# Kernel tuning notes

Hardware: AMD Instinct MI355X
Metric: run time of the kernel (lower is better)

Reference implementation:

```python
import jax, jax.numpy as jnp
import numpy as np

N_NODES = 500_000
N_EDGES = 16_000_000


def setup_inputs() -> dict:
    key = jax.random.key(0)
    ks = jax.random.split(key, 16)
    x = jax.random.normal(ks[0], (N_NODES, 4), dtype=jnp.float32)
    edge_index = jax.random.randint(ks[1], (2, N_EDGES), 0, N_NODES, dtype=jnp.int64)

    def lin(k, out_dim, in_dim):
        # kaiming-uniform-ish init like torch Linear
        bound = 1.0 / np.sqrt(in_dim)
        return jax.random.uniform(k, (out_dim, in_dim), jnp.float32, -bound, bound)

    def bias(k, out_dim, in_dim):
        bound = 1.0 / np.sqrt(in_dim)
        return jax.random.uniform(k, (out_dim,), jnp.float32, -bound, bound)

    return {
        "x": x,
        "edge_index": edge_index,
        # SAGEConv1: 4 -> 10  (lin_l acts on aggregated neighbors, has bias; lin_r on self, no bias)
        "w1l": lin(ks[2], 10, 4), "b1": bias(ks[3], 10, 4), "w1r": lin(ks[4], 10, 4),
        # SAGEConv2: 10 -> 20
        "w2l": lin(ks[5], 20, 10), "b2": bias(ks[6], 20, 10), "w2r": lin(ks[7], 20, 10),
        # SAGEConv3: 20 -> 20
        "w3l": lin(ks[8], 20, 20), "b3": bias(ks[9], 20, 20), "w3r": lin(ks[10], 20, 20),
        # classifier: 20 -> 8
        "wc": lin(ks[11], 8, 20), "bc": bias(ks[12], 8, 20),
    }


def _sage_conv(h, src, dst, deg_inv, wl, bl, wr):
    # mean-aggregate neighbor features: messages flow src -> dst
    msg = h[src]                                   # [E, F] gather
    agg = jax.ops.segment_sum(msg, dst, num_segments=N_NODES)  # [N, F]
    agg = agg * deg_inv                            # mean over in-neighbors
    return agg @ wl.T + bl + h @ wr.T              # lin_l(aggr) + lin_r(self)


def reference(x, edge_index, w1l, b1, w1r, w2l, b2, w2r, w3l, b3, w3r, wc, bc):
    src, dst = edge_index[0], edge_index[1]
    deg = jax.ops.segment_sum(jnp.ones((src.shape[0],), x.dtype), dst,
                              num_segments=N_NODES)
    deg_inv = (1.0 / jnp.maximum(deg, 1.0))[:, None]  # [N, 1]

    h = jax.nn.relu(_sage_conv(x, src, dst, deg_inv, w1l, b1, w1r))
    h = jax.nn.relu(_sage_conv(h, src, dst, deg_inv, w2l, b2, w2r))
    h = jax.nn.relu(_sage_conv(h, src, dst, deg_inv, w3l, b3, w3r))
    return h @ wc.T + bc
```

## Files before the change

kernel.cpp:

```cpp
#include <hip/hip_runtime.h>
#include <hip/hip_fp16.h>

#define N_NODES 500000
#define N_EDGES 16000000
#define NB 1954
#define NPB_LOG 9
#define NPB 512
#define NBUCK 977
#define NBUCK_PAD 1024
#define CH 32768
#define NSB 489

#define SLICE_SHIFT 15
#define NSLICE 16
#define NKEY (NPB * NSLICE)

#define GRID_BLK 1024
#define HALF_T (GRID_BLK * 256)

#define BAR_SUBC 16
#define BAR_SUBQ (GRID_BLK / BAR_SUBC)
#define BAR_REC_INTS 1024
#define BAR_MASTER 512
#define BAR_FLAG 544
#define ENTRY_BUDGET 1500
#define PHASE_BUDGET 400

__device__ __forceinline__ float2 up2(int p) {
    __half2 h = *reinterpret_cast<__half2*>(&p);
    return __half22float2(h);
}
__device__ __forceinline__ int pk2(float a, float b) {
    __half2 h = __floats2half2_rn(a, b);
    return *reinterpret_cast<int*>(&h);
}

__device__ __forceinline__ void barrier_arrive(int* rec, int bid) {
    int r = __hip_atomic_fetch_add(&rec[(bid & (BAR_SUBC - 1)) * 32], 1,
                                   __ATOMIC_RELAXED, __HIP_MEMORY_SCOPE_AGENT);
    if (r == BAR_SUBQ - 1) {
        int mr = __hip_atomic_fetch_add(&rec[BAR_MASTER], 1,
                                        __ATOMIC_RELAXED, __HIP_MEMORY_SCOPE_AGENT);
        if (mr == BAR_SUBC - 1)
            __hip_atomic_store(&rec[BAR_FLAG], 1,
                               __ATOMIC_RELAXED, __HIP_MEMORY_SCOPE_AGENT);
    }
}
__device__ __forceinline__ bool barrier_wait(int* rec, int budget) {
    int spins = 0;
    while (__hip_atomic_load(&rec[BAR_FLAG],
                             __ATOMIC_RELAXED, __HIP_MEMORY_SCOPE_AGENT) == 0) {
        if (++spins > budget) return false;
        __builtin_amdgcn_s_sleep(8);
    }
    return true;
}


__global__ void bucket_hist(const int* __restrict__ dst, int* __restrict__ ghist) {
    __shared__ int lhist[NBUCK_PAD];
    for (int t = threadIdx.x; t < NBUCK_PAD; t += 256) lhist[t] = 0;
    __syncthreads();
    int stride = gridDim.x * 256;
    for (int i = blockIdx.x * 256 + threadIdx.x; i < N_EDGES; i += stride) {
        atomicAdd(&lhist[dst[i] >> NPB_LOG], 1);
    }
    __syncthreads();
    for (int t = threadIdx.x; t < NBUCK_PAD; t += 256) {
        int c = lhist[t];
        if (c) atomicAdd(&ghist[t], c);
    }
}

__global__ void bucket_scan(int* __restrict__ gcur, int* __restrict__ bbase) {
    __shared__ int s[256];
    int t = threadIdx.x;
    int v[4], sum = 0, loc[4];
#pragma unroll
    for (int j = 0; j < 4; ++j) {
        v[j] = gcur[t * 4 + j];
        loc[j] = sum;
        sum += v[j];
    }
    s[t] = sum;
    __syncthreads();
    for (int o = 1; o < 256; o <<= 1) {
        int x = (t >= o) ? s[t - o] : 0;
        __syncthreads();
        s[t] += x;
        __syncthreads();
    }
    int excl = s[t] - sum;
#pragma unroll
    for (int j = 0; j < 4; ++j) {
        int e = excl + loc[j];
        bbase[t * 4 + j] = e;
        gcur[t * 4 + j] = e;
    }
    if (t == 255) bbase[NBUCK_PAD] = s[255];
}

__global__ void bucket_scatter(const int* __restrict__ src, const int* __restrict__ dst,
                               int* __restrict__ gcur, int* __restrict__ P) {
    __shared__ int lhist[NBUCK_PAD];
    __shared__ int lcur[NBUCK_PAD];
    for (int t = threadIdx.x; t < NBUCK_PAD; t += 256) lhist[t] = 0;
    __syncthreads();
    int e0 = blockIdx.x * CH;
    int e1 = min(e0 + CH, N_EDGES);
    for (int i = e0 + threadIdx.x; i < e1; i += 256) {
        atomicAdd(&lhist[dst[i] >> NPB_LOG], 1);
    }
    __syncthreads();
    for (int t = threadIdx.x; t < NBUCK_PAD; t += 256) {
        int c = lhist[t];
        lcur[t] = c ? atomicAdd(&gcur[t], c) : 0;
    }
    __syncthreads();
    for (int i = e0 + threadIdx.x; i < e1; i += 256) {
        int d = dst[i];
        int s = src[i];
        int b = d >> NPB_LOG;
        int pos = atomicAdd(&lcur[b], 1);
        P[pos] = ((d & (NPB - 1)) << 19) | s;
    }
}

__global__ void fine_sort(const int* __restrict__ P, const int* __restrict__ bbase,
                          int* __restrict__ off, int* __restrict__ S) {
    __shared__ int hist[NKEY];
    __shared__ int sscan[256];
    int t = threadIdx.x;
    int b = blockIdx.x;
    int bb = bbase[b];
    int be = bbase[b + 1];
    int node0 = b << NPB_LOG;

    for (int j = t; j < NKEY; j += 256) hist[j] = 0;
    __syncthreads();
    for (int j = bb + t; j < be; j += 256) {
        int p = P[j];
        int n = p >> 19;
        int s = p & 0x7FFFF;
        atomicAdd(&hist[(n << 4) | (s >> SLICE_SHIFT)], 1);
    }
    __syncthreads();

    int base = t * 32;
    int sum = 0;
#pragma unroll
    for (int j = 0; j < 32; ++j) sum += hist[base + j];
    sscan[t] = sum;
    __syncthreads();
    for (int o = 1; o < 256; o <<= 1) {
        int x = (t >= o) ? sscan[t - o] : 0;
        __syncthreads();
        sscan[t] += x;
        __syncthreads();
    }
    int run = sscan[t] - sum;
#pragma unroll
    for (int j = 0; j < 32; ++j) {
        int c = hist[base + j];
        hist[base + j] = run;
        run += c;
    }
    __syncthreads();

#pragma unroll
    for (int j = 0; j < 2; ++j) {
        int idx = t + j * 256;
        int ng = node0 + idx;
        if (ng < N_NODES) off[ng] = bb + hist[idx << 4];
    }
    if (b == NBUCK - 1 && t == 0) off[N_NODES] = N_EDGES;
    __syncthreads();

    for (int j = bb + t; j < be; j += 256) {
        int p = P[j];
        int n = p >> 19;
        int s = p & 0x7FFFF;
        int pos = atomicAdd(&hist[(n << 4) | (s >> SLICE_SHIFT)], 1);
        S[bb + pos] = s;
    }
}

__global__ __launch_bounds__(256) void count_slices(const int* __restrict__ off,
        const int* __restrict__ S, int4* __restrict__ cnt8) {
    int i = blockIdx.x * 256 + threadIdx.x;
    if (i >= N_NODES) return;
    int b = off[i], e = off[i + 1];
    int w0 = 0, w1 = 0, w2 = 0, w3 = 0;
    for (int k = b; k < e; ++k) {
        int sl = S[k] >> SLICE_SHIFT;
        int inc = 1 << ((sl & 3) * 8);
        if (sl < 8) { if (sl < 4) w0 += inc; else w1 += inc; }
        else        { if (sl < 12) w2 += inc; else w3 += inc; }
    }
    cnt8[i] = make_int4(w0, w1, w2, w3);
}


__global__ void convert_x(const float* __restrict__ x, int2* __restrict__ xh) {
    int i = blockIdx.x * 256 + threadIdx.x;
    if (i >= N_NODES) return;
    float4 v = ((const float4*)x)[i];
    int2 r;
    r.x = pk2(v.x, v.y);
    r.y = pk2(v.z, v.w);
    xh[i] = r;
}


__global__ __launch_bounds__(256, 4) void fused_l1(
        const int* __restrict__ off, const int* __restrict__ ssrc,
        const int2* __restrict__ xh, const float* __restrict__ x,
        const float* __restrict__ wl, const float* __restrict__ bl,
        const float* __restrict__ wr, int* __restrict__ h1) {
    __shared__ float s_wl[40];
    __shared__ float s_wr[40];
    __shared__ float s_b[10];
    if (threadIdx.x < 40) {
        s_wl[threadIdx.x] = wl[threadIdx.x];
        s_wr[threadIdx.x] = wr[threadIdx.x];
    }
    if (threadIdx.x >= 64 && threadIdx.x < 74) s_b[threadIdx.x - 64] = bl[threadIdx.x - 64];
    __syncthreads();

    int i = blockIdx.x * 256 + threadIdx.x;
    if (i >= N_NODES) return;

    int b = off[i], e = off[i + 1];
    constexpr int UN = 8;

    float acc[4] = {0.f, 0.f, 0.f, 0.f};

    int k = b;
    for (; k + UN - 1 < e; k += UN) {
        int sidx[UN];
#pragma unroll
        for (int u = 0; u < UN; ++u) sidx[u] = ssrc[k + u];
        int2 v[UN];
#pragma unroll
        for (int u = 0; u < UN; ++u) v[u] = xh[sidx[u]];
#pragma unroll
        for (int u = 0; u < UN; ++u) {
            float2 f0 = up2(v[u].x), f1 = up2(v[u].y);
            acc[0] += f0.x; acc[1] += f0.y; acc[2] += f1.x; acc[3] += f1.y;
        }
    }
    for (; k < e; ++k) {
        int2 v = xh[ssrc[k]];
        float2 f0 = up2(v.x), f1 = up2(v.y);
        acc[0] += f0.x; acc[1] += f0.y; acc[2] += f1.x; acc[3] += f1.y;
    }

    float inv = 1.f / fmaxf((float)(e - b), 1.f);
#pragma unroll
    for (int q = 0; q < 4; ++q) acc[q] *= inv;

    float4 xs = ((const float4*)x)[i];
    float xv[4] = {xs.x, xs.y, xs.z, xs.w};

    float r[10];
#pragma unroll
    for (int j = 0; j < 10; ++j) {
        float t = s_b[j];
#pragma unroll
        for (int kk = 0; kk < 4; ++kk) {
            t += s_wl[j * 4 + kk] * acc[kk] + s_wr[j * 4 + kk] * xv[kk];
        }
        r[j] = fmaxf(t, 0.f);
    }
    int4 o0;
    o0.x = pk2(r[0], r[1]); o0.y = pk2(r[2], r[3]);
    o0.z = pk2(r[4], r[5]); o0.w = pk2(r[6], r[7]);
    *(int4*)(h1 + (long)i * 8) = o0;
    h1[(long)i * 8 + 4] = pk2(r[8], r[9]);
}


__device__ __forceinline__ void l2_scan_m(int& k, int m,
        const int* __restrict__ ssrc, const int* __restrict__ h1, float* acc) {
    for (; m >= 4; m -= 4, k += 4) {
        int sidx[4];
#pragma unroll
        for (int u = 0; u < 4; ++u) sidx[u] = ssrc[k + u];
        int4 v4[4];
        int v1[4];
#pragma unroll
        for (int u = 0; u < 4; ++u) {
            const int* row = h1 + (long)sidx[u] * 8;
            v4[u] = *(const int4*)row;
            v1[u] = row[4];
        }
#pragma unroll
        for (int u = 0; u < 4; ++u) {
            float2 f0 = up2(v4[u].x), f1 = up2(v4[u].y), f2 = up2(v4[u].z),
                   f3 = up2(v4[u].w), f4 = up2(v1[u]);
            acc[0] += f0.x; acc[1] += f0.y; acc[2] += f1.x; acc[3] += f1.y;
            acc[4] += f2.x; acc[5] += f2.y; acc[6] += f3.x; acc[7] += f3.y;
            acc[8] += f4.x; acc[9] += f4.y;
        }
    }
    for (; m > 0; --m, ++k) {
        const int* row = h1 + (long)ssrc[k] * 8;
        int4 v4 = *(const int4*)row;
        int v1 = row[4];
        float2 f0 = up2(v4.x), f1 = up2(v4.y), f2 = up2(v4.z), f3 = up2(v4.w), f4 = up2(v1);
        acc[0] += f0.x; acc[1] += f0.y; acc[2] += f1.x; acc[3] += f1.y;
        acc[4] += f2.x; acc[5] += f2.y; acc[6] += f3.x; acc[7] += f3.y;
        acc[8] += f4.x; acc[9] += f4.y;
    }
}

__device__ __forceinline__ void l3_scan_m(int& k, int m,
        const int* __restrict__ ssrc, const int* __restrict__ h2, float* acc) {
    for (; m >= 4; m -= 4, k += 4) {
        int sidx[4];
#pragma unroll
        for (int u = 0; u < 4; ++u) sidx[u] = ssrc[k + u];
        int4 va[4], vb[4];
        int2 vc[4];
#pragma unroll
        for (int u = 0; u < 4; ++u) {
            const int* row = h2 + (long)sidx[u] * 16;
            va[u] = *(const int4*)row;
            vb[u] = *(const int4*)(row + 4);
            vc[u] = *(const int2*)(row + 8);
        }
#pragma unroll
        for (int u = 0; u < 4; ++u) {
            float2 f;
            f = up2(va[u].x); acc[0] += f.x; acc[1] += f.y;
            f = up2(va[u].y); acc[2] += f.x; acc[3] += f.y;
            f = up2(va[u].z); acc[4] += f.x; acc[5] += f.y;
            f = up2(va[u].w); acc[6] += f.x; acc[7] += f.y;
            f = up2(vb[u].x); acc[8] += f.x; acc[9] += f.y;
            f = up2(vb[u].y); acc[10] += f.x; acc[11] += f.y;
            f = up2(vb[u].z); acc[12] += f.x; acc[13] += f.y;
            f = up2(vb[u].w); acc[14] += f.x; acc[15] += f.y;
            f = up2(vc[u].x); acc[16] += f.x; acc[17] += f.y;
            f = up2(vc[u].y); acc[18] += f.x; acc[19] += f.y;
        }
    }
    for (; m > 0; --m, ++k) {
        const int* row = h2 + (long)ssrc[k] * 16;
        int4 va = *(const int4*)row;
        int4 vb = *(const int4*)(row + 4);
        int2 vc = *(const int2*)(row + 8);
        float2 f;
        f = up2(va.x); acc[0] += f.x; acc[1] += f.y;
        f = up2(va.y); acc[2] += f.x; acc[3] += f.y;
        f = up2(va.z); acc[4] += f.x; acc[5] += f.y;
        f = up2(va.w); acc[6] += f.x; acc[7] += f.y;
        f = up2(vb.x); acc[8] += f.x; acc[9] += f.y;
        f = up2(vb.y); acc[10] += f.x; acc[11] += f.y;
        f = up2(vb.z); acc[12] += f.x; acc[13] += f.y;
        f = up2(vb.w); acc[14] += f.x; acc[15] += f.y;
        f = up2(vc.x); acc[16] += f.x; acc[17] += f.y;
        f = up2(vc.y); acc[18] += f.x; acc[19] += f.y;
    }
}

__device__ __forceinline__ void l2_tail(int n, float deg, float* acc,
        const int* __restrict__ h1, const float* s_wl, const float* s_wr,
        const float* s_b, int* __restrict__ h2) {
    if (n >= N_NODES) return;
    float inv = 1.f / fmaxf(deg, 1.f);
#pragma unroll
    for (int q = 0; q < 10; ++q) acc[q] *= inv;
    float xv[10];
    {
        const int* row = h1 + (long)n * 8;
        int4 v4 = *(const int4*)row;
        int v1 = row[4];
        float2 f0 = up2(v4.x), f1 = up2(v4.y), f2 = up2(v4.z), f3 = up2(v4.w), f4 = up2(v1);
        xv[0] = f0.x; xv[1] = f0.y; xv[2] = f1.x; xv[3] = f1.y;
        xv[4] = f2.x; xv[5] = f2.y; xv[6] = f3.x; xv[7] = f3.y;
        xv[8] = f4.x; xv[9] = f4.y;
    }
    float r[20];
#pragma unroll
    for (int j = 0; j < 20; ++j) {
        float t = s_b[j];
#pragma unroll
        for (int kk = 0; kk < 10; ++kk)
            t += s_wl[j * 10 + kk] * acc[kk] + s_wr[j * 10 + kk] * xv[kk];
        r[j] = fmaxf(t, 0.f);
    }
    int* o = h2 + (long)n * 16;
    int4 o0, o1;
    o0.x = pk2(r[0], r[1]);   o0.y = pk2(r[2], r[3]);
    o0.z = pk2(r[4], r[5]);   o0.w = pk2(r[6], r[7]);
    o1.x = pk2(r[8], r[9]);   o1.y = pk2(r[10], r[11]);
    o1.z = pk2(r[12], r[13]); o1.w = pk2(r[14], r[15]);
    *(int4*)o = o0;
    *(int4*)(o + 4) = o1;
    int2 o2;
    o2.x = pk2(r[16], r[17]); o2.y = pk2(r[18], r[19]);
    *(int2*)(o + 8) = o2;
}

__global__ __launch_bounds__(256, 4) void fused_l2p(
        const int* __restrict__ off, const int* __restrict__ ssrc,
        const int* __restrict__ h1,
        const float* __restrict__ wl, const float* __restrict__ bl,
        const float* __restrict__ wr, int* __restrict__ h2,
        const int4* __restrict__ cnt8, int* __restrict__ bar) {
    __shared__ float s_wl[200];
    __shared__ float s_wr[200];
    __shared__ float s_b[20];
    if (threadIdx.x < 200) {
        s_wl[threadIdx.x] = wl[threadIdx.x];
        s_wr[threadIdx.x] = wr[threadIdx.x];
    }
    if (threadIdx.x >= 224 && threadIdx.x < 244) s_b[threadIdx.x - 224] = bl[threadIdx.x - 224];
    __syncthreads();

    const int tg = blockIdx.x * 256 + threadIdx.x;
    const int n0 = tg, n1 = tg + HALF_T;
    int k0 = off[n0];
    float deg0 = (float)(off[n0 + 1] - k0);
    int4 c0 = cnt8[n0];
    int k1 = 0;
    float deg1 = 0.f;
    int4 c1 = make_int4(0, 0, 0, 0);
    if (n1 < N_NODES) {
        k1 = off[n1];
        deg1 = (float)(off[n1 + 1] - k1);
        c1 = cnt8[n1];
    }
    float acc0[10], acc1[10];
#pragma unroll
    for (int q = 0; q < 10; ++q) { acc0[q] = 0.f; acc1[q] = 0.f; }

    bool coop = true;
    if (threadIdx.x == 0) {
        barrier_arrive(bar, blockIdx.x);
        coop = barrier_wait(bar, ENTRY_BUDGET);
    }
    __syncthreads();

    constexpr int PH = 8;
    for (int s = 0; s < PH; ++s) {
        int cw0 = (s < 4) ? ((s < 2) ? c0.x : c0.y) : ((s < 6) ? c0.z : c0.w);
        int cw1 = (s < 4) ? ((s < 2) ? c1.x : c1.y) : ((s < 6) ? c1.z : c1.w);
        int sh = (s & 1) * 16;
        int m0 = ((cw0 >> sh) & 255) + ((cw0 >> (sh + 8)) & 255);
        int m1 = ((cw1 >> sh) & 255) + ((cw1 >> (sh + 8)) & 255);
        l2_scan_m(k0, m0, ssrc, h1, acc0);
        l2_scan_m(k1, m1, ssrc, h1, acc1);
        if (s < PH - 1) {
            if (threadIdx.x == 0) {
                int* rec = bar + (1 + s) * BAR_REC_INTS;
                barrier_arrive(rec, blockIdx.x);
                if (coop) coop = barrier_wait(rec, PHASE_BUDGET);
            }
            __syncthreads();
        }
    }
    l2_tail(n0, deg0, acc0, h1, s_wl, s_wr, s_b, h2);
    l2_tail(n1, deg1, acc1, h1, s_wl, s_wr, s_b, h2);
}

__device__ __forceinline__ void l3_tail(int n, float deg, float* acc,
        const int* __restrict__ h2, const float* s_wl, const float* s_wr,
        const float* s_b, const float* s_wc, const float* s_bc,
        float* __restrict__ out) {
    if (n >= N_NODES) return;
    float inv = 1.f / fmaxf(deg, 1.f);
#pragma unroll
    for (int q = 0; q < 20; ++q) acc[q] *= inv;
    float xv[20];
    {
        const int* row = h2 + (long)n * 16;
        int4 va = *(const int4*)row;
        int4 vb = *(const int4*)(row + 4);
        int2 vc = *(const int2*)(row + 8);
        float2 f;
        f = up2(va.x); xv[0] = f.x; xv[1] = f.y;
        f = up2(va.y); xv[2] = f.x; xv[3] = f.y;
        f = up2(va.z); xv[4] = f.x; xv[5] = f.y;
        f = up2(va.w); xv[6] = f.x; xv[7] = f.y;
        f = up2(vb.x); xv[8] = f.x; xv[9] = f.y;
        f = up2(vb.y); xv[10] = f.x; xv[11] = f.y;
        f = up2(vb.z); xv[12] = f.x; xv[13] = f.y;
        f = up2(vb.w); xv[14] = f.x; xv[15] = f.y;
        f = up2(vc.x); xv[16] = f.x; xv[17] = f.y;
        f = up2(vc.y); xv[18] = f.x; xv[19] = f.y;
    }
    float h3[20];
#pragma unroll
    for (int j = 0; j < 20; ++j) {
        float r = s_b[j];
#pragma unroll
        for (int kk = 0; kk < 20; ++kk)
            r += s_wl[j * 20 + kk] * acc[kk] + s_wr[j * 20 + kk] * xv[kk];
        h3[j] = fmaxf(r, 0.f);
    }
#pragma unroll
    for (int j = 0; j < 8; ++j) {
        float r = s_bc[j];
#pragma unroll
        for (int kk = 0; kk < 20; ++kk) r += s_wc[j * 20 + kk] * h3[kk];
        out[(long)n * 8 + j] = r;
    }
}

__global__ __launch_bounds__(256, 4) void fused_l3p(
        const int* __restrict__ off, const int* __restrict__ ssrc,
        const int* __restrict__ h2,
        const float* __restrict__ w3l, const float* __restrict__ b3,
        const float* __restrict__ w3r,
        const float* __restrict__ wc, const float* __restrict__ bc,
        float* __restrict__ out, const int4* __restrict__ cnt8,
        int* __restrict__ bar) {
    __shared__ float s_wl[400];
    __shared__ float s_wr[400];
    __shared__ float s_b[20];
    __shared__ float s_wc[160];
    __shared__ float s_bc[8];
    for (int t = threadIdx.x; t < 400; t += 256) {
        s_wl[t] = w3l[t];
        s_wr[t] = w3r[t];
    }
    if (threadIdx.x < 160) s_wc[threadIdx.x] = wc[threadIdx.x];
    if (threadIdx.x >= 192 && threadIdx.x < 212) s_b[threadIdx.x - 192] = b3[threadIdx.x - 192];
    if (threadIdx.x >= 224 && threadIdx.x < 232) s_bc[threadIdx.x - 224] = bc[threadIdx.x - 224];
    __syncthreads();

    const int tg = blockIdx.x * 256 + threadIdx.x;
    const int n0 = tg, n1 = tg + HALF_T;
    int k0 = off[n0];
    float deg0 = (float)(off[n0 + 1] - k0);
    int4 c0 = cnt8[n0];
    int k1 = 0;
    float deg1 = 0.f;
    int4 c1 = make_int4(0, 0, 0, 0);
    if (n1 < N_NODES) {
        k1 = off[n1];
        deg1 = (float)(off[n1 + 1] - k1);
        c1 = cnt8[n1];
    }
    float acc0[20], acc1[20];
#pragma unroll
    for (int q = 0; q < 20; ++q) { acc0[q] = 0.f; acc1[q] = 0.f; }

    bool coop = true;
    if (threadIdx.x == 0) {
        barrier_arrive(bar, blockIdx.x);
        coop = barrier_wait(bar, ENTRY_BUDGET);
    }
    __syncthreads();

    constexpr int PH = 16;
    for (int s = 0; s < PH; ++s) {
        int cw0 = (s < 8) ? ((s < 4) ? c0.x : c0.y) : ((s < 12) ? c0.z : c0.w);
        int cw1 = (s < 8) ? ((s < 4) ? c1.x : c1.y) : ((s < 12) ? c1.z : c1.w);
        int sh = (s & 3) * 8;
        int m0 = (cw0 >> sh) & 255;
        int m1 = (cw1 >> sh) & 255;
        l3_scan_m(k0, m0, ssrc, h2, acc0);
        l3_scan_m(k1, m1, ssrc, h2, acc1);
        if (s < PH - 1) {
            if (threadIdx.x == 0) {
                int* rec = bar + (1 + s) * BAR_REC_INTS;
                barrier_arrive(rec, blockIdx.x);
                if (coop) coop = barrier_wait(rec, PHASE_BUDGET);
            }
            __syncthreads();
        }
    }
    l3_tail(n0, deg0, acc0, h2, s_wl, s_wr, s_b, s_wc, s_bc, out);
    l3_tail(n1, deg1, acc1, h2, s_wl, s_wr, s_b, s_wc, s_bc, out);
}


__global__ void deg_kernel(const int* __restrict__ dst, int* __restrict__ deg) {
    int i = blockIdx.x * blockDim.x + threadIdx.x;
    if (i < N_EDGES) atomicAdd(&deg[dst[i]], 1);
}

template <int F>
__global__ void edge_agg(const int* __restrict__ src, const int* __restrict__ dst,
                         const float* __restrict__ h, float* __restrict__ agg) {
    int i = blockIdx.x * blockDim.x + threadIdx.x;
    if (i >= N_EDGES) return;
    int s = src[i];
    int d = dst[i];
    const float* hs = h + (long)s * F;
    float* ad = agg + (long)d * F;
#pragma unroll
    for (int f = 0; f < F; ++f) atomicAdd(&ad[f], hs[f]);
}

template <int FIN, int FOUT>
__global__ void node_apply(const float* __restrict__ agg, const float* __restrict__ hin,
                           const int* __restrict__ deg, const float* __restrict__ wl,
                           const float* __restrict__ bl, const float* __restrict__ wr,
                           float* __restrict__ hout) {
    __shared__ float s_wl[FOUT * FIN];
    __shared__ float s_wr[FOUT * FIN];
    __shared__ float s_b[FOUT];
    for (int t = threadIdx.x; t < FOUT * FIN; t += blockDim.x) {
        s_wl[t] = wl[t];
        s_wr[t] = wr[t];
    }
    for (int t = threadIdx.x; t < FOUT; t += blockDim.x) s_b[t] = bl[t];
    __syncthreads();
    int i = blockIdx.x * blockDim.x + threadIdx.x;
    if (i >= N_NODES) return;
    float inv = 1.0f / fmaxf((float)deg[i], 1.0f);
    float a[FIN], xv[FIN];
#pragma unroll
    for (int kk = 0; kk < FIN; ++kk) {
        a[kk] = agg[(long)i * FIN + kk] * inv;
        xv[kk] = hin[(long)i * FIN + kk];
    }
#pragma unroll
    for (int j = 0; j < FOUT; ++j) {
        float r = s_b[j];
#pragma unroll
        for (int kk = 0; kk < FIN; ++kk) r += s_wl[j * FIN + kk] * a[kk] + s_wr[j * FIN + kk] * xv[kk];
        hout[(long)i * FOUT + j] = fmaxf(r, 0.f);
    }
}

__global__ void node_final_old(const float* __restrict__ agg, const float* __restrict__ hin,
                               const int* __restrict__ deg, const float* __restrict__ w3l,
                               const float* __restrict__ b3, const float* __restrict__ w3r,
                               const float* __restrict__ wc, const float* __restrict__ bc,
                               float* __restrict__ out) {
    __shared__ float s_wl[400];
    __shared__ float s_wr[400];
    __shared__ float s_b[20];
    __shared__ float s_wc[160];
    __shared__ float s_bc[8];
    for (int t = threadIdx.x; t < 400; t += blockDim.x) {
        s_wl[t] = w3l[t];
        s_wr[t] = w3r[t];
    }
    for (int t = threadIdx.x; t < 160; t += blockDim.x) s_wc[t] = wc[t];
    for (int t = threadIdx.x; t < 20; t += blockDim.x) s_b[t] = b3[t];
    for (int t = threadIdx.x; t < 8; t += blockDim.x) s_bc[t] = bc[t];
    __syncthreads();
    int i = blockIdx.x * blockDim.x + threadIdx.x;
    if (i >= N_NODES) return;
    float inv = 1.0f / fmaxf((float)deg[i], 1.0f);
    float a[20], xv[20];
#pragma unroll
    for (int kk = 0; kk < 20; ++kk) {
        a[kk] = agg[(long)i * 20 + kk] * inv;
        xv[kk] = hin[(long)i * 20 + kk];
    }
    float h3[20];
#pragma unroll
    for (int j = 0; j < 20; ++j) {
        float r = s_b[j];
#pragma unroll
        for (int kk = 0; kk < 20; ++kk) r += s_wl[j * 20 + kk] * a[kk] + s_wr[j * 20 + kk] * xv[kk];
        h3[j] = fmaxf(r, 0.f);
    }
#pragma unroll
    for (int j = 0; j < 8; ++j) {
        float r = s_bc[j];
#pragma unroll
        for (int kk = 0; kk < 20; ++kk) r += s_wc[j * 20 + kk] * h3[kk];
        out[(long)i * 8 + j] = r;
    }
}


extern "C" void kernel_launch(void* const* d_in, const int* in_sizes, int n_in,
                              void* d_out, int out_size, void* d_ws, size_t ws_size,
                              hipStream_t stream) {
    const float* x = (const float*)d_in[0];
    const int* ei = (const int*)d_in[1];
    const float* w1l = (const float*)d_in[2];
    const float* b1 = (const float*)d_in[3];
    const float* w1r = (const float*)d_in[4];
    const float* w2l = (const float*)d_in[5];
    const float* b2 = (const float*)d_in[6];
    const float* w2r = (const float*)d_in[7];
    const float* w3l = (const float*)d_in[8];
    const float* b3 = (const float*)d_in[9];
    const float* w3r = (const float*)d_in[10];
    const float* wc = (const float*)d_in[11];
    const float* bc = (const float*)d_in[12];
    float* out = (float*)d_out;

    const int* src = ei;
    const int* dst = ei + N_EDGES;

    const int BT = 256;
    dim3 blk(BT);
    dim3 egrid((N_EDGES + BT - 1) / BT);
    dim3 ngrid(NB);

    const size_t NEED_A = 130008448;

    if (ws_size >= NEED_A) {
        char* ws = (char*)d_ws;
        int* off = (int*)ws;
        int* bbase = (int*)(ws + 2000128);
        int* gcur = (int*)(ws + 2004352);
        int* P = (int*)(ws + 2008448);
        int2* xh = (int2*)(ws + 2008448);
        int* h1 = (int*)(ws + 6008448);
        int* h2 = (int*)(ws + 22008448);
        int* bar2 = (int*)(ws + 54008448);
        int* bar3 = bar2 + 8 * BAR_REC_INTS;
        int4* cnt8 = (int4*)(ws + 54206464);
        int* S = (int*)(ws + 66008448);

        hipMemsetAsync(gcur, 0, NBUCK_PAD * sizeof(int), stream);
        bucket_hist<<<1024, blk, 0, stream>>>(dst, gcur);
        bucket_scan<<<1, blk, 0, stream>>>(gcur, bbase);
        bucket_scatter<<<NSB, blk, 0, stream>>>(src, dst, gcur, P);
        fine_sort<<<NBUCK, blk, 0, stream>>>(P, bbase, off, S);

        hipMemsetAsync(bar2, 0, 24 * BAR_REC_INTS * sizeof(int), stream);

        count_slices<<<ngrid, blk, 0, stream>>>(off, S, cnt8);
        convert_x<<<ngrid, blk, 0, stream>>>(x, xh);
        fused_l1<<<ngrid, blk, 0, stream>>>(off, S, xh, x, w1l, b1, w1r, h1);
        fused_l2p<<<GRID_BLK, blk, 0, stream>>>(off, S, h1, w2l, b2, w2r, h2, cnt8, bar2);
        fused_l3p<<<GRID_BLK, blk, 0, stream>>>(off, S, h2, w3l, b3, w3r, wc, bc, out, cnt8, bar3);
    } else {
        char* ws = (char*)d_ws;
        int* deg = (int*)ws;
        float* agg = (float*)(ws + 2000000);
        float* h1 = (float*)(ws + 42000000);
        float* h2 = (float*)(ws + 62000000);

        hipMemsetAsync(deg, 0, (size_t)N_NODES * sizeof(int), stream);
        deg_kernel<<<egrid, blk, 0, stream>>>(dst, deg);

        hipMemsetAsync(agg, 0, (size_t)N_NODES * 4 * sizeof(float), stream);
        edge_agg<4><<<egrid, blk, 0, stream>>>(src, dst, x, agg);
        node_apply<4, 10><<<ngrid, blk, 0, stream>>>(agg, x, deg, w1l, b1, w1r, h1);

        hipMemsetAsync(agg, 0, (size_t)N_NODES * 10 * sizeof(float), stream);
        edge_agg<10><<<egrid, blk, 0, stream>>>(src, dst, h1, agg);
        node_apply<10, 20><<<ngrid, blk, 0, stream>>>(agg, h1, deg, w2l, b2, w2r, h2);

        hipMemsetAsync(agg, 0, (size_t)N_NODES * 20 * sizeof(float), stream);
        edge_agg<20><<<egrid, blk, 0, stream>>>(src, dst, h2, agg);
        node_final_old<<<ngrid, blk, 0, stream>>>(agg, h2, deg, w3l, b3, w3r, wc, bc, out);
    }
}
```

Before: 1.587 ms.

## Stage bucket scatter in LDS and write contiguous per-bucket runs to global

The bucket scatter kernel now sorts each chunk's edges locally in shared memory, using a block-wide prefix scan over the bucket histogram, and then copies each bucket's run to global memory with one wavefront per bucket. The goal is to replace random 4-byte global writes with mostly contiguous writes. To fit the 64KB staging buffer, the chunk size is halved, which doubles the block count and the number of global atomics on bucket cursors. Runs average only about 16 elements per bucket, so coalescing gains may be limited, and the large LDS footprint lowers occupancy.

```diff
diff --git a/kernel.cpp b/kernel.cpp
--- a/kernel.cpp
+++ b/kernel.cpp
@@ -8,8 +8,8 @@
 #define NPB 512
 #define NBUCK 977
 #define NBUCK_PAD 1024
-#define CH 32768
-#define NSB 489
+#define CH 16384
+#define NSB 977
 
 #define SLICE_SHIFT 15
 #define NSLICE 16
@@ -100,29 +100,67 @@
     if (t == 255) bbase[NBUCK_PAD] = s[255];
 }
 
-__global__ void bucket_scatter(const int* __restrict__ src, const int* __restrict__ dst,
-                               int* __restrict__ gcur, int* __restrict__ P) {
+__global__ __launch_bounds__(256) void bucket_scatter(
+        const int* __restrict__ src, const int* __restrict__ dst,
+        int* __restrict__ gcur, int* __restrict__ P) {
+    __shared__ int lP[CH];
     __shared__ int lhist[NBUCK_PAD];
-    __shared__ int lcur[NBUCK_PAD];
-    for (int t = threadIdx.x; t < NBUCK_PAD; t += 256) lhist[t] = 0;
-    __syncthreads();
+    __shared__ int lexcl[NBUCK_PAD];
+    __shared__ int gbase[NBUCK_PAD];
+    __shared__ int sscan[256];
+    int t = threadIdx.x;
+    for (int j = t; j < NBUCK_PAD; j += 256) lhist[j] = 0;
+    __syncthreads();
+
     int e0 = blockIdx.x * CH;
     int e1 = min(e0 + CH, N_EDGES);
-    for (int i = e0 + threadIdx.x; i < e1; i += 256) {
+    for (int i = e0 + t; i < e1; i += 256) {
         atomicAdd(&lhist[dst[i] >> NPB_LOG], 1);
     }
     __syncthreads();
-    for (int t = threadIdx.x; t < NBUCK_PAD; t += 256) {
-        int c = lhist[t];
-        lcur[t] = c ? atomicAdd(&gcur[t], c) : 0;
-    }
-    __syncthreads();
-    for (int i = e0 + threadIdx.x; i < e1; i += 256) {
+
+    int base4 = t * 4;
+    int c[4], sum = 0;
+#pragma unroll
+    for (int j = 0; j < 4; ++j) { c[j] = lhist[base4 + j]; sum += c[j]; }
+#pragma unroll
+    for (int j = 0; j < 4; ++j) {
+        gbase[base4 + j] = c[j] ? atomicAdd(&gcur[base4 + j], c[j]) : 0;
+    }
+    sscan[t] = sum;
+    __syncthreads();
+    for (int o = 1; o < 256; o <<= 1) {
+        int x = (t >= o) ? sscan[t - o] : 0;
+        __syncthreads();
+        sscan[t] += x;
+        __syncthreads();
+    }
+    int run = sscan[t] - sum;
+#pragma unroll
+    for (int j = 0; j < 4; ++j) {
+        lexcl[base4 + j] = run;
+        lhist[base4 + j] = run;
+        run += c[j];
+    }
+    __syncthreads();
+
+    for (int i = e0 + t; i < e1; i += 256) {
         int d = dst[i];
         int s = src[i];
         int b = d >> NPB_LOG;
-        int pos = atomicAdd(&lcur[b], 1);
-        P[pos] = ((d & (NPB - 1)) << 19) | s;
+        int pos = atomicAdd(&lhist[b], 1);
+        lP[pos] = ((d & (NPB - 1)) << 19) | s;
+    }
+    __syncthreads();
+
+    int wave = t >> 6, lane = t & 63;
+    for (int b = wave; b < NBUCK_PAD; b += 4) {
+        int lb = lexcl[b];
+        int cnt = lhist[b] - lb;
+        int gb = gbase[b];
+        for (int j = lane; j < cnt; j += 64) {
+            P[gb + j] = lP[lb + j];
+        }
     }
 }
 
```

Result: faster. 1.494 ms (-5.8%).
